# Kernel optimization log

Measured on AMD Instinct MI355X. Metric: run time of the kernel, lower is better.

Reference implementation:

```python
import jax, jax.numpy as jnp
import numpy as np

N_NODES = 50000


def setup_inputs() -> dict:
    key = jax.random.key(0)
    k1, k2, k3, k4, k5 = jax.random.split(key, 5)
    F_IN, F_OUT, E = 128, 128, 800000
    x = jax.random.normal(k1, (N_NODES, F_IN), dtype=jnp.float32)
    edge_index = jax.random.randint(k2, (2, E), 0, N_NODES, dtype=jnp.int64)
    # PyG Linear uses Kaiming-ish init; scale for stable magnitudes
    s = 1.0 / np.sqrt(F_IN)
    W_l = jax.random.normal(k3, (F_IN, F_OUT), dtype=jnp.float32) * s
    W_r = jax.random.normal(k4, (F_IN, F_OUT), dtype=jnp.float32) * s
    b = jax.random.normal(k5, (F_OUT,), dtype=jnp.float32) * s
    return {"x": x, "edge_index": edge_index, "W_l": W_l, "W_r": W_r, "b": b}


def reference(x, edge_index, W_l, W_r, b):
    # SAGEConv (mean aggr): out = mean_{j in N(i)} x_j @ W_l + x_i @ W_r + b
    src, dst = edge_index[0], edge_index[1]
    msgs = x[src]  # [E, F_in] gather
    summed = jax.ops.segment_sum(msgs, dst, num_segments=N_NODES)  # [N, F_in]
    deg = jax.ops.segment_sum(jnp.ones_like(dst, dtype=x.dtype), dst,
                              num_segments=N_NODES)  # [N]
    mean = summed / jnp.maximum(deg, 1.0)[:, None]
    return mean @ W_l + x @ W_r + b
```

## Files before the change

### kernel.cpp

```cpp
#include <hip/hip_runtime.h>

#define N_NODES 50000
#define F 128
#define NBIN 98
#define BIN_NODES 512
#define BINCAP 10000
#define CAPN 60
#define NB_A 256
#define NB_CV 6250
#define NB_BT 128

typedef __attribute__((ext_vector_type(8))) short bf16x8;
typedef __attribute__((ext_vector_type(4))) float f32x4;
typedef __attribute__((ext_vector_type(4))) unsigned int u32x4;

__device__ __forceinline__ unsigned short f2bf(float f) {
    unsigned u = __float_as_uint(f);
    unsigned r = u + 0x7FFFu + ((u >> 16) & 1u);
    return (unsigned short)(r >> 16);
}

__global__ __launch_bounds__(128) void init_kernel(int* __restrict__ cursor)
{
    const int t = threadIdx.x;
    if (t < NBIN) cursor[t] = t * BINCAP;
}

__global__ __launch_bounds__(256) void fused_prep_kernel(
    const float* __restrict__ x, unsigned short* __restrict__ xb,
    const int* __restrict__ src, const int* __restrict__ dst,
    int* __restrict__ cursor, unsigned* __restrict__ binbuf,
    const float* __restrict__ Wl, const float* __restrict__ Wr,
    unsigned short* __restrict__ Bt, int E)
{
    const int bid = blockIdx.x;
    const int t = threadIdx.x;

    if (bid < NB_A) {
        __shared__ int hist[NBIN], hist2[NBIN], base[NBIN];
        if (t < NBIN) { hist[t] = 0; hist2[t] = 0; }
        __syncthreads();

        const int e0 = bid * 3125;
        for (int j = t; j < 3125; j += 256)
            atomicAdd(&hist[dst[e0 + j] >> 9], 1);
        __syncthreads();

        if (t < NBIN) base[t] = atomicAdd(&cursor[t], hist[t]);
        __syncthreads();

        for (int j = t; j < 3125; j += 256) {
            const int d = dst[e0 + j];
            const int s = src[e0 + j];
            const int b = d >> 9;
            const int r = atomicAdd(&hist2[b], 1);
            binbuf[base[b] + r] = (unsigned)s | ((unsigned)(d & 511) << 16);
        }
    } else if (bid < NB_A + NB_CV) {
        const int i = (bid - NB_A) * 256 + t;
        const float4 v = reinterpret_cast<const float4*>(x)[i];
        ushort4 o;
        o.x = f2bf(v.x); o.y = f2bf(v.y); o.z = f2bf(v.z); o.w = f2bf(v.w);
        reinterpret_cast<ushort4*>(xb)[i] = o;
    } else {
        const int gid = (bid - NB_A - NB_CV) * 256 + t;
        const int n = gid >> 8;
        const int k = gid & 255;
        const float v = (k < F) ? Wl[k * F + n] : Wr[(k - F) * F + n];
        Bt[gid] = f2bf(v);
    }
}

__global__ __launch_bounds__(512) void binscatter_kernel(
    const unsigned* __restrict__ binbuf, const int* __restrict__ cursor,
    unsigned short* __restrict__ bucket, int* __restrict__ deg)
{
    __shared__ __align__(16) unsigned short lb[BIN_NODES * CAPN];
    __shared__ int degL[BIN_NODES];

    const int b = blockIdx.x, t = threadIdx.x;

    for (int i = t; i < BIN_NODES; i += 512) degL[i] = 0;
    __syncthreads();

    const int lo = b * BINCAP;
    const int hi = cursor[b];
    for (int j = lo + t; j < hi; j += 512) {
        const unsigned p = binbuf[j];
        const int dl = p >> 16;
        const int r = atomicAdd(&degL[dl], 1);
        lb[dl * CAPN + r] = (unsigned short)(p & 0xFFFFu);
    }
    __syncthreads();

    const int gnode0 = b * BIN_NODES;
    for (int i = t; i < BIN_NODES; i += 512) {
        const int gn = gnode0 + i;
        if (gn < N_NODES) deg[gn] = degL[i];
    }
    const unsigned* lb32 = reinterpret_cast<const unsigned*>(lb);
    unsigned* gb32 = reinterpret_cast<unsigned*>(&bucket[(size_t)gnode0 * CAPN]);
    for (int i = t; i < BIN_NODES * CAPN / 2; i += 512) gb32[i] = lb32[i];
}

__global__ __launch_bounds__(256) void agg_out_kernel(
    const unsigned short* __restrict__ xb,
    const unsigned short* __restrict__ bucket,
    const int* __restrict__ deg,
    const unsigned short* __restrict__ Bt,
    const float* __restrict__ bias,
    float* __restrict__ out)
{
    __shared__ __align__(16) unsigned short mean_s[16][136];
    __shared__ float cs[16][132];

    const int t = threadIdx.x;
    const int w = t >> 6, lane = t & 63;
    const int g = lane >> 4, li = lane & 15;
    const int ln = w * 4 + g;
    const int mbase = blockIdx.x * 16;
    const int node = mbase + ln;

    const int cnt_total = deg[node];
    const unsigned short* bkt = &bucket[(size_t)node * CAPN];

    float a0 = 0.f, a1 = 0.f, a2 = 0.f, a3 = 0.f;
    float a4 = 0.f, a5 = 0.f, a6 = 0.f, a7 = 0.f;

    const int colu = li * 8;
    const int gbase = g * 16;

    const int idx0 = (li      < cnt_total) ? (int)bkt[li]      : 0;
    const int idx1 = (li + 16 < cnt_total) ? (int)bkt[li + 16] : 0;
    const int idx2 = (li + 32 < cnt_total) ? (int)bkt[li + 32] : 0;
    const int idx3 = (li + 48 < cnt_total) ? (int)bkt[li + 48] : 0;

#define ACCV(v)                                   \
    {                                             \
        a0 += __uint_as_float((v).x << 16);       \
        a1 += __uint_as_float((v).x & 0xFFFF0000u); \
        a2 += __uint_as_float((v).y << 16);       \
        a3 += __uint_as_float((v).y & 0xFFFF0000u); \
        a4 += __uint_as_float((v).z << 16);       \
        a5 += __uint_as_float((v).z & 0xFFFF0000u); \
        a6 += __uint_as_float((v).w << 16);       \
        a7 += __uint_as_float((v).w & 0xFFFF0000u); \
    }

    for (int j = 0; j < cnt_total; j += 8) {
        const int c = j >> 4;
        int sel = idx0;
        sel = (c == 1) ? idx1 : sel;
        sel = (c == 2) ? idx2 : sel;
        sel = (c == 3) ? idx3 : sel;
        const int o = gbase + (j & 15);
        const int r0 = __shfl(sel, o + 0);
        const int r1 = __shfl(sel, o + 1);
        const int r2 = __shfl(sel, o + 2);
        const int r3 = __shfl(sel, o + 3);
        const int r4 = __shfl(sel, o + 4);
        const int r5 = __shfl(sel, o + 5);
        const int r6 = __shfl(sel, o + 6);
        const int r7 = __shfl(sel, o + 7);
        const u32x4 v0 = *reinterpret_cast<const u32x4*>(&xb[(size_t)r0 * F + colu]);
        const u32x4 v1 = *reinterpret_cast<const u32x4*>(&xb[(size_t)r1 * F + colu]);
        const u32x4 v2 = *reinterpret_cast<const u32x4*>(&xb[(size_t)r2 * F + colu]);
        const u32x4 v3 = *reinterpret_cast<const u32x4*>(&xb[(size_t)r3 * F + colu]);
        const u32x4 v4 = *reinterpret_cast<const u32x4*>(&xb[(size_t)r4 * F + colu]);
        const u32x4 v5 = *reinterpret_cast<const u32x4*>(&xb[(size_t)r5 * F + colu]);
        const u32x4 v6 = *reinterpret_cast<const u32x4*>(&xb[(size_t)r6 * F + colu]);
        const u32x4 v7 = *reinterpret_cast<const u32x4*>(&xb[(size_t)r7 * F + colu]);
        const int rem = cnt_total - j;
        ACCV(v0)
        if (rem > 1) ACCV(v1)
        if (rem > 2) ACCV(v2)
        if (rem > 3) ACCV(v3)
        if (rem > 4) ACCV(v4)
        if (rem > 5) ACCV(v5)
        if (rem > 6) ACCV(v6)
        if (rem > 7) ACCV(v7)
    }
#undef ACCV

    {
        const float inv = (cnt_total > 0) ? (1.0f / (float)cnt_total) : 1.0f;
        u32x4 u;
        u.x = (unsigned)f2bf(a0 * inv) | ((unsigned)f2bf(a1 * inv) << 16);
        u.y = (unsigned)f2bf(a2 * inv) | ((unsigned)f2bf(a3 * inv) << 16);
        u.z = (unsigned)f2bf(a4 * inv) | ((unsigned)f2bf(a5 * inv) << 16);
        u.w = (unsigned)f2bf(a6 * inv) | ((unsigned)f2bf(a7 * inv) << 16);
        *reinterpret_cast<u32x4*>(&mean_s[ln][colu]) = u;
    }
    __syncthreads();

    const int arow = mbase + li;
    const int kchunk = g * 8;

    bf16x8 a[8];
#pragma unroll
    for (int s = 0; s < 4; ++s) {
        a[s] = *reinterpret_cast<const bf16x8*>(&mean_s[li][s * 32 + kchunk]);
        a[s + 4] = *reinterpret_cast<const bf16x8*>(
            &xb[(size_t)arow * F + s * 32 + kchunk]);
    }

    f32x4 acc[2];
    acc[0] = (f32x4){0.f, 0.f, 0.f, 0.f};
    acc[1] = (f32x4){0.f, 0.f, 0.f, 0.f};

#pragma unroll
    for (int s = 0; s < 8; ++s) {
#pragma unroll
        for (int nt = 0; nt < 2; ++nt) {
            const bf16x8 bf = *reinterpret_cast<const bf16x8*>(
                &Bt[(size_t)((w * 2 + nt) * 16 + li) * 256 + s * 32 + kchunk]);
            acc[nt] = __builtin_amdgcn_mfma_f32_16x16x32_bf16(a[s], bf, acc[nt], 0, 0, 0);
        }
    }

#pragma unroll
    for (int nt = 0; nt < 2; ++nt) {
        const int col = (w * 2 + nt) * 16 + li;
        const float bv = bias[col];
#pragma unroll
        for (int r = 0; r < 4; ++r)
            cs[g * 4 + r][col] = acc[nt][r] + bv;
    }
    __syncthreads();

#pragma unroll
    for (int i = 0; i < 2; ++i) {
        const int idx = t + i * 256;
        const int r = idx >> 5;
        const int c4 = (idx & 31) << 2;
        float4 v;
        v.x = cs[r][c4 + 0];
        v.y = cs[r][c4 + 1];
        v.z = cs[r][c4 + 2];
        v.w = cs[r][c4 + 3];
        *reinterpret_cast<float4*>(&out[(size_t)(mbase + r) * F + c4]) = v;
    }
}

extern "C" void kernel_launch(void* const* d_in, const int* in_sizes, int n_in,
                              void* d_out, int out_size, void* d_ws, size_t ws_size,
                              hipStream_t stream)
{
    const float* x  = (const float*)d_in[0];
    const int*   ei = (const int*)d_in[1];
    const float* Wl = (const float*)d_in[2];
    const float* Wr = (const float*)d_in[3];
    const float* b  = (const float*)d_in[4];
    float* out = (float*)d_out;

    const int E = in_sizes[1] / 2;
    const int* src = ei;
    const int* dst = ei + E;

    int* cursor = (int*)d_ws;
    int* deg    = cursor + 128;
    unsigned* binbuf = (unsigned*)(deg + 50176);
    unsigned short* bucket = (unsigned short*)(binbuf + 980000);
    unsigned short* xb     = bucket + (size_t)NBIN * BIN_NODES * CAPN;
    unsigned short* Bt     = xb + (size_t)N_NODES * F;

    init_kernel<<<1, 128, 0, stream>>>(cursor);

    fused_prep_kernel<<<NB_A + NB_CV + NB_BT, 256, 0, stream>>>(
        x, xb, src, dst, cursor, binbuf, Wl, Wr, Bt, E);

    binscatter_kernel<<<NBIN, 512, 0, stream>>>(binbuf, cursor, bucket, deg);

    agg_out_kernel<<<N_NODES / 16, 256, 0, stream>>>(
        xb, bucket, deg, Bt, b, out);
}
```

Baseline: 86.59 us.

## Replace fixed-capacity per-node buckets with compact CSR and halve agg block size

The binscatter kernel now counts per-node degrees, prefix-sums them within each bin and across bins, and writes a compact CSR neighbor array plus per-node start offsets. This replaces the fixed 60-slot-per-node bucket layout, removing the padded global writes and the per-node cap. The aggregation/output kernel now handles 8 nodes per 128-thread block, so each MFMA pass uses only half of its 16 rows (the rest are zero-padded) and each wave computes four output tiles. The intent is to cut bucket memory traffic and raise block count and occupancy, at the cost of an extra pass over binbuf, more prefix-sum synchronization, and wasted MFMA rows.

```diff
diff --git a/kernel.cpp b/kernel.cpp
--- a/kernel.cpp
+++ b/kernel.cpp
@@ -5,7 +5,6 @@
 #define NBIN 98
 #define BIN_NODES 512
 #define BINCAP 10000
-#define CAPN 60
 #define NB_A 256
 #define NB_CV 6250
 #define NB_BT 128
@@ -73,56 +72,98 @@
 
 __global__ __launch_bounds__(512) void binscatter_kernel(
     const unsigned* __restrict__ binbuf, const int* __restrict__ cursor,
-    unsigned short* __restrict__ bucket, int* __restrict__ deg)
-{
-    __shared__ __align__(16) unsigned short lb[BIN_NODES * CAPN];
-    __shared__ int degL[BIN_NODES];
+    unsigned short* __restrict__ csr, int* __restrict__ start,
+    int* __restrict__ deg)
+{
+    __shared__ int degL[BIN_NODES], lofs[BIN_NODES], cnt2[BIN_NODES];
+    __shared__ unsigned short lbc[BINCAP];
+    __shared__ int wsumS[8];
+    __shared__ int pre[128];
+    __shared__ int cbaseS;
 
     const int b = blockIdx.x, t = threadIdx.x;
-
-    for (int i = t; i < BIN_NODES; i += 512) degL[i] = 0;
-    __syncthreads();
-
+    const int lane = t & 63, wid = t >> 6;
+
+    degL[t] = 0; cnt2[t] = 0;
+    if (t < 128) {
+        int v = (t < NBIN) ? (cursor[t] - t * BINCAP) : 0;
+        int incl = v;
+#pragma unroll
+        for (int off = 1; off < 64; off <<= 1) {
+            const int u = __shfl_up(incl, off, 64);
+            if (lane >= off) incl += u;
+        }
+        pre[t] = incl;
+    }
+    __syncthreads();
+    if (t == 0)
+        cbaseS = (b == 0) ? 0 : ((b <= 64) ? pre[b - 1]
+                                           : pre[63] + pre[b - 1]);
     const int lo = b * BINCAP;
     const int hi = cursor[b];
+    const int n = hi - lo;
+
+    for (int j = lo + t; j < hi; j += 512)
+        atomicAdd(&degL[binbuf[j] >> 16], 1);
+    __syncthreads();
+
+    {
+        const int v = degL[t];
+        int incl = v;
+#pragma unroll
+        for (int off = 1; off < 64; off <<= 1) {
+            const int u = __shfl_up(incl, off, 64);
+            if (lane >= off) incl += u;
+        }
+        if (lane == 63) wsumS[wid] = incl;
+        __syncthreads();
+        if (t == 0) {
+            int run = 0;
+#pragma unroll
+            for (int w = 0; w < 8; ++w) { const int s = wsumS[w]; wsumS[w] = run; run += s; }
+        }
+        __syncthreads();
+        lofs[t] = wsumS[wid] + incl - v;
+    }
+    __syncthreads();
+
     for (int j = lo + t; j < hi; j += 512) {
         const unsigned p = binbuf[j];
         const int dl = p >> 16;
-        const int r = atomicAdd(&degL[dl], 1);
-        lb[dl * CAPN + r] = (unsigned short)(p & 0xFFFFu);
-    }
-    __syncthreads();
-
-    const int gnode0 = b * BIN_NODES;
-    for (int i = t; i < BIN_NODES; i += 512) {
-        const int gn = gnode0 + i;
-        if (gn < N_NODES) deg[gn] = degL[i];
-    }
-    const unsigned* lb32 = reinterpret_cast<const unsigned*>(lb);
-    unsigned* gb32 = reinterpret_cast<unsigned*>(&bucket[(size_t)gnode0 * CAPN]);
-    for (int i = t; i < BIN_NODES * CAPN / 2; i += 512) gb32[i] = lb32[i];
-}
-
-__global__ __launch_bounds__(256) void agg_out_kernel(
+        const int r = atomicAdd(&cnt2[dl], 1);
+        lbc[lofs[dl] + r] = (unsigned short)(p & 0xFFFFu);
+    }
+    __syncthreads();
+
+    const int gn0 = b * BIN_NODES;
+    if (gn0 + t < N_NODES) {
+        start[gn0 + t] = cbaseS + lofs[t];
+        deg[gn0 + t] = degL[t];
+    }
+    for (int i = t; i < n; i += 512) csr[cbaseS + i] = lbc[i];
+}
+
+__global__ __launch_bounds__(128) void agg_out_kernel(
     const unsigned short* __restrict__ xb,
-    const unsigned short* __restrict__ bucket,
+    const unsigned short* __restrict__ csr,
+    const int* __restrict__ start,
     const int* __restrict__ deg,
     const unsigned short* __restrict__ Bt,
     const float* __restrict__ bias,
     float* __restrict__ out)
 {
-    __shared__ __align__(16) unsigned short mean_s[16][136];
-    __shared__ float cs[16][132];
+    __shared__ __align__(16) unsigned short mean_s[8][136];
+    __shared__ float cs[8][132];
 
     const int t = threadIdx.x;
     const int w = t >> 6, lane = t & 63;
     const int g = lane >> 4, li = lane & 15;
-    const int ln = w * 4 + g;
-    const int mbase = blockIdx.x * 16;
-    const int node = mbase + ln;
+    const int gg = w * 4 + g;
+    const int mbase = blockIdx.x * 8;
+    const int node = mbase + gg;
 
     const int cnt_total = deg[node];
-    const unsigned short* bkt = &bucket[(size_t)node * CAPN];
+    const int s0 = start[node];
 
     float a0 = 0.f, a1 = 0.f, a2 = 0.f, a3 = 0.f;
     float a4 = 0.f, a5 = 0.f, a6 = 0.f, a7 = 0.f;
@@ -130,10 +171,10 @@
     const int colu = li * 8;
     const int gbase = g * 16;
 
-    const int idx0 = (li      < cnt_total) ? (int)bkt[li]      : 0;
-    const int idx1 = (li + 16 < cnt_total) ? (int)bkt[li + 16] : 0;
-    const int idx2 = (li + 32 < cnt_total) ? (int)bkt[li + 32] : 0;
-    const int idx3 = (li + 48 < cnt_total) ? (int)bkt[li + 48] : 0;
+    const int idx0 = (li      < cnt_total) ? (int)csr[s0 + li]      : 0;
+    const int idx1 = (li + 16 < cnt_total) ? (int)csr[s0 + li + 16] : 0;
+    const int idx2 = (li + 32 < cnt_total) ? (int)csr[s0 + li + 32] : 0;
+    const int idx3 = (li + 48 < cnt_total) ? (int)csr[s0 + li + 48] : 0;
 
 #define ACCV(v)                                   \
     {                                             \
@@ -189,48 +230,56 @@
         u.y = (unsigned)f2bf(a2 * inv) | ((unsigned)f2bf(a3 * inv) << 16);
         u.z = (unsigned)f2bf(a4 * inv) | ((unsigned)f2bf(a5 * inv) << 16);
         u.w = (unsigned)f2bf(a6 * inv) | ((unsigned)f2bf(a7 * inv) << 16);
-        *reinterpret_cast<u32x4*>(&mean_s[ln][colu]) = u;
-    }
-    __syncthreads();
-
-    const int arow = mbase + li;
+        *reinterpret_cast<u32x4*>(&mean_s[gg][colu]) = u;
+    }
+    __syncthreads();
+
     const int kchunk = g * 8;
+    const bool rok = li < 8;
+    const int lrow = li & 7;
 
     bf16x8 a[8];
 #pragma unroll
     for (int s = 0; s < 4; ++s) {
-        a[s] = *reinterpret_cast<const bf16x8*>(&mean_s[li][s * 32 + kchunk]);
-        a[s + 4] = *reinterpret_cast<const bf16x8*>(
-            &xb[(size_t)arow * F + s * 32 + kchunk]);
-    }
-
-    f32x4 acc[2];
-    acc[0] = (f32x4){0.f, 0.f, 0.f, 0.f};
-    acc[1] = (f32x4){0.f, 0.f, 0.f, 0.f};
+        a[s]     = (bf16x8){0, 0, 0, 0, 0, 0, 0, 0};
+        a[s + 4] = (bf16x8){0, 0, 0, 0, 0, 0, 0, 0};
+        if (rok) {
+            a[s] = *reinterpret_cast<const bf16x8*>(
+                &mean_s[lrow][s * 32 + kchunk]);
+            a[s + 4] = *reinterpret_cast<const bf16x8*>(
+                &xb[(size_t)(mbase + lrow) * F + s * 32 + kchunk]);
+        }
+    }
+
+    f32x4 acc[4];
+#pragma unroll
+    for (int nt = 0; nt < 4; ++nt) acc[nt] = (f32x4){0.f, 0.f, 0.f, 0.f};
 
 #pragma unroll
     for (int s = 0; s < 8; ++s) {
 #pragma unroll
-        for (int nt = 0; nt < 2; ++nt) {
+        for (int nt = 0; nt < 4; ++nt) {
             const bf16x8 bf = *reinterpret_cast<const bf16x8*>(
-                &Bt[(size_t)((w * 2 + nt) * 16 + li) * 256 + s * 32 + kchunk]);
+                &Bt[(size_t)((w * 4 + nt) * 16 + li) * 256 + s * 32 + kchunk]);
             acc[nt] = __builtin_amdgcn_mfma_f32_16x16x32_bf16(a[s], bf, acc[nt], 0, 0, 0);
         }
     }
 
 #pragma unroll
-    for (int nt = 0; nt < 2; ++nt) {
-        const int col = (w * 2 + nt) * 16 + li;
+    for (int nt = 0; nt < 4; ++nt) {
+        const int col = (w * 4 + nt) * 16 + li;
         const float bv = bias[col];
 #pragma unroll
-        for (int r = 0; r < 4; ++r)
-            cs[g * 4 + r][col] = acc[nt][r] + bv;
+        for (int r = 0; r < 4; ++r) {
+            const int crow = g * 4 + r;
+            if (crow < 8) cs[crow][col] = acc[nt][r] + bv;
+        }
     }
     __syncthreads();
 
 #pragma unroll
     for (int i = 0; i < 2; ++i) {
-        const int idx = t + i * 256;
+        const int idx = t + i * 128;
         const int r = idx >> 5;
         const int c4 = (idx & 31) << 2;
         float4 v;
@@ -258,19 +307,20 @@
     const int* dst = ei + E;
 
     int* cursor = (int*)d_ws;
-    int* deg    = cursor + 128;
+    int* start  = cursor + 128;
+    int* deg    = start + 50176;
     unsigned* binbuf = (unsigned*)(deg + 50176);
-    unsigned short* bucket = (unsigned short*)(binbuf + 980000);
-    unsigned short* xb     = bucket + (size_t)NBIN * BIN_NODES * CAPN;
-    unsigned short* Bt     = xb + (size_t)N_NODES * F;
+    unsigned short* csr = (unsigned short*)(binbuf + 980000);
+    unsigned short* xb  = csr + 800064;
+    unsigned short* Bt  = xb + (size_t)N_NODES * F;
 
     init_kernel<<<1, 128, 0, stream>>>(cursor);
 
     fused_prep_kernel<<<NB_A + NB_CV + NB_BT, 256, 0, stream>>>(
         x, xb, src, dst, cursor, binbuf, Wl, Wr, Bt, E);
 
-    binscatter_kernel<<<NBIN, 512, 0, stream>>>(binbuf, cursor, bucket, deg);
-
-    agg_out_kernel<<<N_NODES / 16, 256, 0, stream>>>(
-        xb, bucket, deg, Bt, b, out);
-}
+    binscatter_kernel<<<NBIN, 512, 0, stream>>>(binbuf, cursor, csr, start, deg);
+
+    agg_out_kernel<<<N_NODES / 8, 128, 0, stream>>>(
+        xb, csr, start, deg, Bt, b, out);
+}
```

Measured after the change: 111.1 us. +28.3%, slower.
